# Kernel tuning notes

Hardware: AMD Instinct MI355X
Metric: run time of the kernel (lower is better)

The kernel has to match this reference:

```python
import jax, jax.numpy as jnp
import numpy as np

B, L, H, TD = 384, 64, 300, 64   # batch, seq_len, encoder_size, tracking_lstm_dim
T = 2 * (L - 1)                  # L-1 shifts interleaved with L-1 reduces (valid tree)


def setup_inputs() -> dict:
    key = jax.random.key(0)
    ks = jax.random.split(key, 9)

    def w(k, shape):
        fan_in = shape[-1]
        return jax.random.normal(k, shape, jnp.float32) * (2.0 / fan_in) ** 0.5

    sequence = jax.random.normal(ks[0], (B, L, 2 * H), jnp.float32)
    # valid transition sequences: odd steps shift (1), even steps reduce left(2)/right(3)
    rng = np.random.default_rng(0)
    tr = np.empty((B, T), dtype=np.int32)
    tr[:, 0::2] = 1
    tr[:, 1::2] = rng.integers(2, 4, size=(B, T // 2))
    return {
        "sequence": sequence,
        "transitions": jnp.asarray(tr),
        # DependencyTreeLSTMCell params (5 gates each)
        "W_c": w(ks[1], (5 * H, TD)),    # input (tracking) -> gates, no bias
        "Uh_w": w(ks[2], (5 * H, H)),    # U_head (with bias)
        "Uh_b": jnp.zeros((5 * H,), jnp.float32),
        "Ul_w": w(ks[3], (5 * H, H)),    # U_child_left, no bias
        "Ur_w": w(ks[4], (5 * H, H)),    # U_child_right, no bias
        # tracking nn.LSTMCell params (torch gate order i,f,g,o)
        "W_ih": w(ks[5], (4 * TD, 3 * H)),
        "W_hh": w(ks[6], (4 * TD, TD)),
        "b_ih": jnp.zeros((4 * TD,), jnp.float32),
        "b_hh": jnp.zeros((4 * TD,), jnp.float32),
        # original code initializes the tracking state with torch.randn
        "th0": jax.random.normal(ks[7], (B, TD), jnp.float32),
        "tc0": jax.random.normal(ks[8], (B, TD), jnp.float32),
    }


def _encode(sequence, transitions, W_c, Uh_w, Uh_b, Ul_w, Ur_w,
            W_ih, W_hh, b_ih, b_hh, th0, tc0):
    Bz, Lz, D2 = sequence.shape
    Hz = D2 // 2
    tokens_h, tokens_c = sequence[..., :Hz], sequence[..., Hz:]
    bidx = jnp.arange(Bz)
    S = Lz + 1  # max stack depth
    stack_h = jnp.zeros((Bz, S, Hz), sequence.dtype)
    stack_h = stack_h.at[:, 0].set(tokens_h[:, 0]).at[:, 1].set(tokens_h[:, 0])
    stack_c = jnp.zeros((Bz, S, Hz), sequence.dtype)
    stack_c = stack_c.at[:, 0].set(tokens_c[:, 0]).at[:, 1].set(tokens_c[:, 0])
    sp = jnp.full((Bz,), 2, jnp.int32)   # stack pointer (stack seeded with token 0 twice)
    bp = jnp.zeros((Bz,), jnp.int32)     # buffer pointer (buffer NOT popped by the seed)

    def step(carry, trans):
        stack_h, stack_c, sp, bp, th, tc = carry
        buf_h = tokens_h[bidx, bp]
        buf_c = tokens_c[bidx, bp]
        s1_h = stack_h[bidx, sp - 1]
        s2_h = stack_h[bidx, sp - 2]
        s1_c = stack_c[bidx, sp - 1]
        s2_c = stack_c[bidx, sp - 2]
        # tracking LSTMCell on [buffer_top, stack_top, stack_second]
        x = jnp.concatenate([buf_h, s1_h, s2_h], axis=1)          # (B, 3H)
        g = x @ W_ih.T + b_ih + th @ W_hh.T + b_hh                # (B, 4*TD)
        i_t, f_t, g_t, o_t = jnp.split(g, 4, axis=1)
        tc = jax.nn.sigmoid(f_t) * tc + jax.nn.sigmoid(i_t) * jnp.tanh(g_t)
        th = jax.nn.sigmoid(o_t) * jnp.tanh(tc)
        # composition. NOTE: the original cell does `h_child, c_child = hc_head`,
        # so only the HEAD state enters the gate math -- replicated faithfully.
        is_left = trans == 2
        is_red = is_left | (trans == 3)
        lm = is_left[:, None]
        h_head = jnp.where(lm, s1_h, s2_h)   # left-arc: head is the stack top
        c_head = jnp.where(lm, s1_c, s2_c)
        u_dir = jnp.where(lm, h_head @ Ul_w.T, h_head @ Ur_w.T)
        gates = h_head @ Uh_w.T + Uh_b + u_dir + th @ W_c.T       # (B, 5H)
        i_j, o_j, f_jh, f_jc, u_j = jnp.split(gates, 5, axis=1)
        c_j = (jax.nn.sigmoid(i_j) * jnp.tanh(u_j)
               + jax.nn.sigmoid(f_jh) * c_head
               + jax.nn.sigmoid(f_jc) * c_head)  # c_child aliases c_head in original
        h_j = jax.nn.sigmoid(o_j) * jnp.tanh(c_j)
        # stack update: shift pushes buffer top at sp; reduce pops 2, writes at sp-2
        rm = is_red[:, None]
        wpos = jnp.where(is_red, sp - 2, sp)
        stack_h = stack_h.at[bidx, wpos].set(jnp.where(rm, h_j, buf_h))
        stack_c = stack_c.at[bidx, wpos].set(jnp.where(rm, c_j, buf_c))
        sp = jnp.where(is_red, sp - 1, sp + 1)
        bp = bp + (trans == 1).astype(bp.dtype)
        return (stack_h, stack_c, sp, bp, th, tc), None

    init = (stack_h, stack_c, sp, bp, th0, tc0)
    (stack_h, stack_c, sp, bp, th, tc), _ = jax.lax.scan(step, init, transitions.T)
    return stack_h[bidx, sp - 1]   # (B, H): hidden state of each stack top


def reference(sequence, transitions, W_c, Uh_w, Uh_b, Ul_w, Ur_w,
              W_ih, W_hh, b_ih, b_hh, th0, tc0):
    return _encode(sequence, transitions, W_c, Uh_w, Uh_b, Ul_w, Ur_w,
                   W_ih, W_hh, b_ih, b_hh, th0, tc0)
```

## Files before the change

### kernel.cpp

```cpp
#include <hip/hip_runtime.h>
#include <stdint.h>

#define BB 384
#define LSEQ 64
#define HH 300
#define TDIM 64
#define TT 126
#define NP 63
#define KP 320
#define G4 256
#define G5 1500
#define SEQB 38400

typedef unsigned int u32;
typedef unsigned short ush;
typedef float f32x4 __attribute__((ext_vector_type(4)));
typedef short bf16x8 __attribute__((ext_vector_type(8)));

__device__ __forceinline__ float sigm(float x){ return 1.0f/(1.0f + expf(-x)); }
__device__ __forceinline__ ush f2bf(float x){ u32 u = __float_as_uint(x); u32 r = u + 0x7fff + ((u>>16)&1); return (ush)(r>>16); }
__device__ __forceinline__ float bf2f(ush h){ return __uint_as_float(((u32)h)<<16); }
__device__ __forceinline__ bf16x8 ld16(const ush* p){ return *reinterpret_cast<const bf16x8*>(p); }
__device__ __forceinline__ void mfma16(f32x4& d, bf16x8 a, bf16x8 b){
    d = __builtin_amdgcn_mfma_f32_16x16x32_bf16(a, b, d, 0, 0, 0);
}

__global__ void k_wprep(const float* __restrict__ Uh, const float* __restrict__ Ul,
                        const float* __restrict__ Ur, const float* __restrict__ Wih,
                        const float* __restrict__ Whh,
                        const float* __restrict__ bih, const float* __restrict__ bhh,
                        ush* ULh, ush* ULl, ush* URh, ush* URl,
                        ush* WihH, ush* WihL, ush* WhhH, ush* WhhL, float* bsum)
{
    int i0 = blockIdx.x*blockDim.x + threadIdx.x;
    int stride = gridDim.x*blockDim.x;
    for (int i = i0; i < G5*KP; i += stride) {
        int j = i / KP, k = i - j*KP;
        float vl = 0.f, vr = 0.f;
        if (k < HH) { float u = Uh[j*HH+k]; vl = u + Ul[j*HH+k]; vr = u + Ur[j*HH+k]; }
        ush h;
        h = f2bf(vl); ULh[i] = h; ULl[i] = f2bf(vl - bf2f(h));
        h = f2bf(vr); URh[i] = h; URl[i] = f2bf(vr - bf2f(h));
    }
    for (int i = i0; i < G4*3*KP; i += stride) {
        int j = i / (3*KP), kk = i - j*(3*KP);
        int part = kk / KP, k = kk - part*KP;
        float v = (k < HH) ? Wih[j*900 + part*HH + k] : 0.f;
        ush h = f2bf(v); WihH[i] = h; WihL[i] = f2bf(v - bf2f(h));
    }
    for (int i = i0; i < G4*TDIM; i += stride) {
        float v = Whh[i]; ush h = f2bf(v); WhhH[i] = h; WhhL[i] = f2bf(v - bf2f(h));
    }
    for (int i = i0; i < G4; i += stride) bsum[i] = bih[i] + bhh[i];
}

__global__ void k_cvt(const float* __restrict__ seq, ush* tokH, ush* tokL)
{
    int i0 = blockIdx.x*blockDim.x + threadIdx.x;
    int stride = gridDim.x*blockDim.x;
    for (int i = i0; i < BB*LSEQ*KP; i += stride) {
        int bt = i / KP, k = i - bt*KP;
        int b = bt >> 6, t = bt & 63;
        float v = (k < HH) ? seq[b*SEQB + t*600 + k] : 0.f;
        ush h = f2bf(v); tokH[i] = h; tokL[i] = f2bf(v - bf2f(h));
    }
}

__global__ void k_init(const float* __restrict__ seq, const float* __restrict__ th0,
                       const float* __restrict__ tc0, const ush* __restrict__ tokH,
                       const ush* __restrict__ tokL,
                       ush* accH, ush* accL, float* acc_c, float* acc_h,
                       ush* thH, ush* thL, float* tc_buf)
{
    int i0 = blockIdx.x*blockDim.x + threadIdx.x;
    int stride = gridDim.x*blockDim.x;
    for (int i = i0; i < BB*KP; i += stride) {
        int b = i / KP, k = i - b*KP;
        accH[i] = tokH[b*LSEQ*KP + k]; accL[i] = tokL[b*LSEQ*KP + k];
    }
    for (int i = i0; i < BB*HH; i += stride) {
        int b = i / HH, c = i - b*HH;
        acc_c[i] = seq[b*SEQB + HH + c];
        acc_h[i] = seq[b*SEQB + c];
    }
    for (int i = i0; i < BB*TDIM; i += stride) {
        float v = th0[i]; ush h = f2bf(v);
        thH[i] = h; thL[i] = f2bf(v - bf2f(h));
        tc_buf[i] = tc0[i];
    }
}

__global__ __launch_bounds__(448) void k_prep2(const int* __restrict__ trans, int* perm, int* rbarr)
{
    int p = blockIdx.x, t = threadIdx.x;
    __shared__ int cl, cr, rb;
    if (t == 0) { cl = 0; cr = 0; }
    __syncthreads();
    int isleft = 0;
    if (t < BB) {
        isleft = (trans[t*TT + 2*p + 1] == 2);
        if (isleft) atomicAdd(&cl, 1); else atomicAdd(&cr, 1);
    }
    __syncthreads();
    if (t == 0) { rb = ((cl + 63) >> 6) << 6; rbarr[p] = rb; cl = 0; cr = 0; }
    __syncthreads();
    perm[p*448 + t] = -1;
    __syncthreads();
    if (t < BB) {
        int slot = isleft ? atomicAdd(&cl, 1) : rb + atomicAdd(&cr, 1);
        perm[p*448 + slot] = t;
    }
}

__global__ __launch_bounds__(256) void k_pairA(int p,
    const ush* __restrict__ tokH, const ush* __restrict__ tokL,
    const ush* __restrict__ accHp, const ush* __restrict__ accLp,
    const ush* __restrict__ thHp, const ush* __restrict__ thLp,
    const ush* __restrict__ ULh, const ush* __restrict__ ULl,
    const ush* __restrict__ URh, const ush* __restrict__ URl,
    const ush* __restrict__ WihH, const ush* __restrict__ WihL,
    const ush* __restrict__ WhhH, const ush* __restrict__ WhhL,
    const int* __restrict__ perm, const int* __restrict__ rbarr,
    float* __restrict__ gbufE, float* __restrict__ gbufO, float* __restrict__ Pbuf)
{
    const int bid = blockIdx.x, tid = threadIdx.x;
    const int w = tid >> 6, lane = tid & 63;
    const int l15 = lane & 15, kg = lane >> 4;
    f32x4 acc[4];
    #pragma unroll
    for (int cf = 0; cf < 4; ++cf) acc[cf] = (f32x4){0.f,0.f,0.f,0.f};

    if (bid < 48) {
        const int seg = (bid >= 24);
        const int q = bid - seg*24;
        const int rt = q >> 2, ct = q & 3;
        const int r0 = rt*64, c0 = ct*64;
        const int b = r0 + w*16 + l15;
        const ush* aH[3]; const ush* aL[3];
        if (!seg) {
            aH[0] = tokH + (b*64 + p)*KP;   aL[0] = tokL + (b*64 + p)*KP;
            aH[1] = accHp + b*KP;           aL[1] = accLp + b*KP;
            aH[2] = tokH + (b*64)*KP;       aL[2] = tokL + (b*64)*KP;
        } else {
            aH[0] = tokH + (b*64 + p+1)*KP; aL[0] = tokL + (b*64 + p+1)*KP;
            aH[1] = tokH + (b*64 + p)*KP;   aL[1] = tokL + (b*64 + p)*KP;
            aH[2] = accHp + b*KP;           aL[2] = accLp + b*KP;
        }
        const ush* bH[4]; const ush* bL[4];
        #pragma unroll
        for (int cf = 0; cf < 4; ++cf) {
            int j = c0 + cf*16 + l15;
            bH[cf] = WihH + j*(3*KP) + kg*8;
            bL[cf] = WihL + j*(3*KP) + kg*8;
        }
        #pragma unroll
        for (int part = 0; part < 3; ++part) {
            const ush* pah = aH[part] + kg*8;
            const ush* pal = aL[part] + kg*8;
            const int ko = part*KP;
            #pragma unroll
            for (int kc = 0; kc < KP; kc += 32) {
                bf16x8 ah = ld16(pah + kc);
                bf16x8 al = ld16(pal + kc);
                bf16x8 b0 = ld16(bH[0]+ko+kc), b1 = ld16(bH[1]+ko+kc), b2 = ld16(bH[2]+ko+kc), b3 = ld16(bH[3]+ko+kc);
                bf16x8 c0v = ld16(bL[0]+ko+kc), c1 = ld16(bL[1]+ko+kc), c2 = ld16(bL[2]+ko+kc), c3 = ld16(bL[3]+ko+kc);
                mfma16(acc[0],ah,b0); mfma16(acc[1],ah,b1); mfma16(acc[2],ah,b2); mfma16(acc[3],ah,b3);
                mfma16(acc[0],al,b0); mfma16(acc[1],al,b1); mfma16(acc[2],al,b2); mfma16(acc[3],al,b3);
                mfma16(acc[0],ah,c0v); mfma16(acc[1],ah,c1); mfma16(acc[2],ah,c2); mfma16(acc[3],ah,c3);
            }
        }
        if (!seg) {
            const ush* pah = thHp + b*TDIM + kg*8;
            const ush* pal = thLp + b*TDIM + kg*8;
            #pragma unroll
            for (int kc = 0; kc < 64; kc += 32) {
                bf16x8 ah = ld16(pah + kc);
                bf16x8 al = ld16(pal + kc);
                #pragma unroll
                for (int cf = 0; cf < 4; ++cf) {
                    int j = c0 + cf*16 + l15;
                    bf16x8 bh = ld16(WhhH + j*TDIM + kg*8 + kc);
                    bf16x8 bl = ld16(WhhL + j*TDIM + kg*8 + kc);
                    mfma16(acc[cf], ah, bh);
                    mfma16(acc[cf], al, bh);
                    mfma16(acc[cf], ah, bl);
                }
            }
        }
        float* out = seg ? gbufO : gbufE;
        #pragma unroll
        for (int r = 0; r < 4; ++r) {
            int row = r0 + w*16 + kg*4 + r;
            #pragma unroll
            for (int cf = 0; cf < 4; ++cf) {
                int col = c0 + cf*16 + l15;
                out[row*G4 + col] = acc[cf][r];
            }
        }
    } else {
        const int q = bid - 48;
        const int rt = q / 24, ct = q - rt*24;
        const int s0 = rt*64, c0 = ct*64;
        const int* pp = perm + p*448;
        if (pp[s0] < 0) return;
        const int RB = rbarr[p];
        const bool left = (s0 < RB);
        int ar = pp[s0 + w*16 + l15]; if (ar < 0) ar = 0;
        const ush* pah = (left ? tokH + (ar*64 + p)*KP : accHp + ar*KP) + kg*8;
        const ush* pal = (left ? tokL + (ar*64 + p)*KP : accLp + ar*KP) + kg*8;
        const ush* WBh = left ? ULh : URh;
        const ush* WBl = left ? ULl : URl;
        const ush* bH[4]; const ush* bL[4];
        #pragma unroll
        for (int cf = 0; cf < 4; ++cf) {
            int j = c0 + cf*16 + l15; if (j > G5-1) j = G5-1;
            bH[cf] = WBh + j*KP + kg*8;
            bL[cf] = WBl + j*KP + kg*8;
        }
        #pragma unroll
        for (int kc = 0; kc < KP; kc += 32) {
            bf16x8 ah = ld16(pah + kc);
            bf16x8 al = ld16(pal + kc);
            bf16x8 b0 = ld16(bH[0]+kc), b1 = ld16(bH[1]+kc), b2 = ld16(bH[2]+kc), b3 = ld16(bH[3]+kc);
            bf16x8 c0v = ld16(bL[0]+kc), c1 = ld16(bL[1]+kc), c2 = ld16(bL[2]+kc), c3 = ld16(bL[3]+kc);
            mfma16(acc[0],ah,b0); mfma16(acc[1],ah,b1); mfma16(acc[2],ah,b2); mfma16(acc[3],ah,b3);
            mfma16(acc[0],al,b0); mfma16(acc[1],al,b1); mfma16(acc[2],al,b2); mfma16(acc[3],al,b3);
            mfma16(acc[0],ah,c0v); mfma16(acc[1],ah,c1); mfma16(acc[2],ah,c2); mfma16(acc[3],ah,c3);
        }
        #pragma unroll
        for (int r = 0; r < 4; ++r) {
            int pr = pp[s0 + w*16 + kg*4 + r];
            if (pr < 0) continue;
            #pragma unroll
            for (int cf = 0; cf < 4; ++cf) {
                int col = c0 + cf*16 + l15;
                if (col < G5) Pbuf[pr*G5 + col] = acc[cf][r];
            }
        }
    }
}

__global__ __launch_bounds__(256) void k_pairB(int p,
    const float* __restrict__ seq, const int* __restrict__ trans,
    const float* __restrict__ Whh, const float* __restrict__ Wc,
    const float* __restrict__ Uhb, const float* __restrict__ bsum,
    const float* __restrict__ gbufE, const float* __restrict__ gbufO,
    const float* __restrict__ Pbuf,
    ush* __restrict__ thH, ush* __restrict__ thL, float* __restrict__ tc_buf,
    float* __restrict__ acc_c, float* __restrict__ acc_h,
    ush* __restrict__ accHp, ush* __restrict__ accLp)
{
    __shared__ __align__(16) float thl[4][64], tcl[4][64], gel[4][256];
    __shared__ __align__(16) float g5l[4][G5];
    const int tid = threadIdx.x;
    const int r0 = blockIdx.x*4;
    const int row = tid >> 6, d = tid & 63;
    const int b = r0 + row;

    {
        float gi = gbufE[b*G4 + d]        + bsum[d];
        float gf = gbufE[b*G4 + 64 + d]   + bsum[64 + d];
        float gg = gbufE[b*G4 + 128 + d]  + bsum[128 + d];
        float go = gbufE[b*G4 + 192 + d]  + bsum[192 + d];
        float tcp = tc_buf[b*TDIM + d];
        float tce = sigm(gf)*tcp + sigm(gi)*tanhf(gg);
        float the = sigm(go)*tanhf(tce);
        thl[row][d] = the; tcl[row][d] = tce;
    }
    __syncthreads();
    {
        int j = tid;
        float s[4] = {0.f,0.f,0.f,0.f};
        #pragma unroll
        for (int k = 0; k < 64; k += 4) {
            float4 wv = *(const float4*)&Whh[j*TDIM + k];
            #pragma unroll
            for (int rr = 0; rr < 4; ++rr) {
                float4 t4 = *(const float4*)&thl[rr][k];
                s[rr] += t4.x*wv.x + t4.y*wv.y + t4.z*wv.z + t4.w*wv.w;
            }
        }
        float bs = bsum[j];
        #pragma unroll
        for (int rr = 0; rr < 4; ++rr)
            gel[rr][j] = gbufO[(r0+rr)*G4 + j] + bs + s[rr];
    }
    __syncthreads();
    {
        float gi = gel[row][d], gf = gel[row][64+d], gg = gel[row][128+d], go = gel[row][192+d];
        float tco = sigm(gf)*tcl[row][d] + sigm(gi)*tanhf(gg);
        float tho = sigm(go)*tanhf(tco);
        tc_buf[b*TDIM + d] = tco;
        ush h = f2bf(tho);
        thH[b*TDIM + d] = h; thL[b*TDIM + d] = f2bf(tho - bf2f(h));
        __syncthreads();
        thl[row][d] = tho;
    }
    __syncthreads();
    for (int c = tid; c < G5; c += 256) {
        float s[4] = {0.f,0.f,0.f,0.f};
        #pragma unroll
        for (int k = 0; k < 64; k += 4) {
            float4 wv = *(const float4*)&Wc[c*TDIM + k];
            #pragma unroll
            for (int rr = 0; rr < 4; ++rr) {
                float4 t4 = *(const float4*)&thl[rr][k];
                s[rr] += t4.x*wv.x + t4.y*wv.y + t4.z*wv.z + t4.w*wv.w;
            }
        }
        float ub = Uhb[c];
        #pragma unroll
        for (int rr = 0; rr < 4; ++rr)
            g5l[rr][c] = Pbuf[(r0+rr)*G5 + c] + ub + s[rr];
    }
    __syncthreads();
    for (int idx = tid; idx < 4*HH; idx += 256) {
        int rr = idx / HH, c = idx - rr*HH;
        int bb = r0 + rr;
        bool left = (trans[bb*TT + 2*p + 1] == 2);
        float ch = left ? seq[bb*SEQB + p*600 + HH + c] : acc_c[bb*HH + c];
        float gi = g5l[rr][c], go = g5l[rr][HH+c], gfh = g5l[rr][2*HH+c], gfc = g5l[rr][3*HH+c], gu = g5l[rr][4*HH+c];
        float cj = sigm(gi)*tanhf(gu) + (sigm(gfh) + sigm(gfc))*ch;
        float hj = sigm(go)*tanhf(cj);
        acc_c[bb*HH + c] = cj;
        acc_h[bb*HH + c] = hj;
        ush h = f2bf(hj);
        accHp[bb*KP + c] = h; accLp[bb*KP + c] = f2bf(hj - bf2f(h));
    }
}

__global__ void k_out(const float* __restrict__ acc_h, float* __restrict__ out)
{
    int i = blockIdx.x*blockDim.x + threadIdx.x;
    if (i < BB*HH) out[i] = acc_h[i];
}

extern "C" void kernel_launch(void* const* d_in, const int* in_sizes, int n_in,
                              void* d_out, int out_size, void* d_ws, size_t ws_size,
                              hipStream_t stream)
{
    const float* seq  = (const float*)d_in[0];
    const int*   trans= (const int*)d_in[1];
    const float* Wc   = (const float*)d_in[2];
    const float* Uhw  = (const float*)d_in[3];
    const float* Uhb  = (const float*)d_in[4];
    const float* Ulw  = (const float*)d_in[5];
    const float* Urw  = (const float*)d_in[6];
    const float* Wih  = (const float*)d_in[7];
    const float* Whh  = (const float*)d_in[8];
    const float* bih  = (const float*)d_in[9];
    const float* bhh  = (const float*)d_in[10];
    const float* th0  = (const float*)d_in[11];
    const float* tc0  = (const float*)d_in[12];
    float* out = (float*)d_out;

    char* w = (char*)d_ws;
    size_t off = 0;
    auto alloc = [&](size_t nbytes) {
        void* ptr = w + off;
        off = (off + nbytes + 255) & ~(size_t)255;
        return ptr;
    };
    ush* tokH = (ush*)alloc((size_t)BB*LSEQ*KP*2);
    ush* tokL = (ush*)alloc((size_t)BB*LSEQ*KP*2);
    ush* accH = (ush*)alloc((size_t)BB*KP*2);
    ush* accL = (ush*)alloc((size_t)BB*KP*2);
    ush* ULh  = (ush*)alloc((size_t)G5*KP*2);
    ush* ULl  = (ush*)alloc((size_t)G5*KP*2);
    ush* URh  = (ush*)alloc((size_t)G5*KP*2);
    ush* URl  = (ush*)alloc((size_t)G5*KP*2);
    ush* WihH = (ush*)alloc((size_t)G4*3*KP*2);
    ush* WihL = (ush*)alloc((size_t)G4*3*KP*2);
    ush* WhhH = (ush*)alloc((size_t)G4*TDIM*2);
    ush* WhhL = (ush*)alloc((size_t)G4*TDIM*2);
    ush* thH  = (ush*)alloc((size_t)BB*TDIM*2);
    ush* thL  = (ush*)alloc((size_t)BB*TDIM*2);
    float* bsum  = (float*)alloc((size_t)G4*4);
    float* gbufE = (float*)alloc((size_t)BB*G4*4);
    float* gbufO = (float*)alloc((size_t)BB*G4*4);
    float* Pbuf  = (float*)alloc((size_t)BB*G5*4);
    float* tcb   = (float*)alloc((size_t)BB*TDIM*4);
    float* acc_c = (float*)alloc((size_t)BB*HH*4);
    float* acc_h = (float*)alloc((size_t)BB*HH*4);
    int* perm  = (int*)alloc((size_t)NP*448*4);
    int* rbarr = (int*)alloc((size_t)NP*4);

    k_wprep<<<960, 256, 0, stream>>>(Uhw, Ulw, Urw, Wih, Whh, bih, bhh,
                                     ULh, ULl, URh, URl, WihH, WihL, WhhH, WhhL, bsum);
    k_cvt<<<2048, 256, 0, stream>>>(seq, tokH, tokL);
    k_init<<<512, 256, 0, stream>>>(seq, th0, tc0, tokH, tokL,
                                    accH, accL, acc_c, acc_h, thH, thL, tcb);
    k_prep2<<<NP, 448, 0, stream>>>(trans, perm, rbarr);

    for (int p = 0; p < NP; ++p) {
        k_pairA<<<216, 256, 0, stream>>>(p, tokH, tokL, accH, accL, thH, thL,
                                         ULh, ULl, URh, URl, WihH, WihL, WhhH, WhhL,
                                         perm, rbarr, gbufE, gbufO, Pbuf);
        k_pairB<<<96, 256, 0, stream>>>(p, seq, trans, Whh, Wc, Uhb, bsum,
                                        gbufE, gbufO, Pbuf,
                                        thH, thL, tcb, acc_c, acc_h, accH, accL);
    }
    k_out<<<(BB*HH + 255)/256, 256, 0, stream>>>(acc_h, out);
}
```

Baseline: 4.255 ms.

## Fuse per-step kernel pairs into one persistent kernel with grid barriers

Replaces the 126 per-step kernel launches (pairA/pairB for each of 63 pairs) with a single persistent kernel of 216 blocks that loops over steps and synchronises with an atomic-counter grid barrier. The aim is to remove launch overhead and inter-kernel gaps on the sequential recurrence. The risk is that it relies on all 216 blocks being co-resident, and spin-wait barriers add their own latency. Shared memory for the elementwise phase is now allocated in every block, which may reduce occupancy.

```diff
diff --git a/kernel.cpp b/kernel.cpp
--- a/kernel.cpp
+++ b/kernel.cpp
@@ -11,6 +11,7 @@
 #define G4 256
 #define G5 1500
 #define SEQB 38400
+#define NBLK 216
 
 typedef unsigned int u32;
 typedef unsigned short ush;
@@ -23,6 +24,18 @@
 __device__ __forceinline__ bf16x8 ld16(const ush* p){ return *reinterpret_cast<const bf16x8*>(p); }
 __device__ __forceinline__ void mfma16(f32x4& d, bf16x8 a, bf16x8 b){
     d = __builtin_amdgcn_mfma_f32_16x16x32_bf16(a, b, d, 0, 0, 0);
+}
+
+__device__ __forceinline__ void gbar(int* cnt, int target) {
+    __syncthreads();
+    if (threadIdx.x == 0) {
+        __threadfence();
+        __hip_atomic_fetch_add(cnt, 1, __ATOMIC_RELEASE, __HIP_MEMORY_SCOPE_AGENT);
+        while (__hip_atomic_load(cnt, __ATOMIC_ACQUIRE, __HIP_MEMORY_SCOPE_AGENT) < target)
+            __builtin_amdgcn_s_sleep(2);
+        __threadfence();
+    }
+    __syncthreads();
 }
 
 __global__ void k_wprep(const float* __restrict__ Uh, const float* __restrict__ Ul,
@@ -90,9 +103,11 @@
     }
 }
 
-__global__ __launch_bounds__(448) void k_prep2(const int* __restrict__ trans, int* perm, int* rbarr)
+__global__ __launch_bounds__(448) void k_prep2(const int* __restrict__ trans, int* perm, int* rbarr,
+                                               int* bar)
 {
     int p = blockIdx.x, t = threadIdx.x;
+    if (p == 0 && t == 0) *bar = 0;
     __shared__ int cl, cr, rb;
     if (t == 0) { cl = 0; cr = 0; }
     __syncthreads();
@@ -112,220 +127,227 @@
     }
 }
 
-__global__ __launch_bounds__(256) void k_pairA(int p,
-    const ush* __restrict__ tokH, const ush* __restrict__ tokL,
-    const ush* __restrict__ accHp, const ush* __restrict__ accLp,
-    const ush* __restrict__ thHp, const ush* __restrict__ thLp,
-    const ush* __restrict__ ULh, const ush* __restrict__ ULl,
-    const ush* __restrict__ URh, const ush* __restrict__ URl,
-    const ush* __restrict__ WihH, const ush* __restrict__ WihL,
-    const ush* __restrict__ WhhH, const ush* __restrict__ WhhL,
-    const int* __restrict__ perm, const int* __restrict__ rbarr,
-    float* __restrict__ gbufE, float* __restrict__ gbufO, float* __restrict__ Pbuf)
+struct Prm {
+    const float* seq; const int* trans;
+    const float* Wc; const float* Uhb; const float* bsum;
+    const ush* tokH; const ush* tokL;
+    ush* accH; ush* accL;
+    ush* thH; ush* thL;
+    float* tcb; float* acc_c; float* acc_h;
+    const ush* ULh; const ush* ULl; const ush* URh; const ush* URl;
+    const ush* WihH; const ush* WihL; const ush* WhhH; const ush* WhhL;
+    const float* Whh;
+    const int* perm; const int* rbarr;
+    float* gbufE; float* gbufO; float* Pbuf;
+    int* bar;
+};
+
+__global__ __launch_bounds__(256) void k_persist(Prm pr)
 {
     const int bid = blockIdx.x, tid = threadIdx.x;
     const int w = tid >> 6, lane = tid & 63;
     const int l15 = lane & 15, kg = lane >> 4;
-    f32x4 acc[4];
-    #pragma unroll
-    for (int cf = 0; cf < 4; ++cf) acc[cf] = (f32x4){0.f,0.f,0.f,0.f};
-
-    if (bid < 48) {
-        const int seg = (bid >= 24);
-        const int q = bid - seg*24;
-        const int rt = q >> 2, ct = q & 3;
-        const int r0 = rt*64, c0 = ct*64;
-        const int b = r0 + w*16 + l15;
-        const ush* aH[3]; const ush* aL[3];
-        if (!seg) {
-            aH[0] = tokH + (b*64 + p)*KP;   aL[0] = tokL + (b*64 + p)*KP;
-            aH[1] = accHp + b*KP;           aL[1] = accLp + b*KP;
-            aH[2] = tokH + (b*64)*KP;       aL[2] = tokL + (b*64)*KP;
-        } else {
-            aH[0] = tokH + (b*64 + p+1)*KP; aL[0] = tokL + (b*64 + p+1)*KP;
-            aH[1] = tokH + (b*64 + p)*KP;   aL[1] = tokL + (b*64 + p)*KP;
-            aH[2] = accHp + b*KP;           aL[2] = accLp + b*KP;
-        }
-        const ush* bH[4]; const ush* bL[4];
-        #pragma unroll
-        for (int cf = 0; cf < 4; ++cf) {
-            int j = c0 + cf*16 + l15;
-            bH[cf] = WihH + j*(3*KP) + kg*8;
-            bL[cf] = WihL + j*(3*KP) + kg*8;
-        }
-        #pragma unroll
-        for (int part = 0; part < 3; ++part) {
-            const ush* pah = aH[part] + kg*8;
-            const ush* pal = aL[part] + kg*8;
-            const int ko = part*KP;
+
+    __shared__ __align__(16) float thl[4][64], tcl[4][64], gel[4][256];
+    __shared__ __align__(16) float g5l[4][G5];
+
+    int btgt = 0;
+    for (int p = 0; p < NP; ++p) {
+        if (bid < 48) {
+            const int seg = (bid >= 24);
+            const int q = bid - seg*24;
+            const int rt = q >> 2, ct = q & 3;
+            const int r0 = rt*64, c0 = ct*64;
+            const int b = r0 + w*16 + l15;
+            f32x4 acc[4];
             #pragma unroll
-            for (int kc = 0; kc < KP; kc += 32) {
-                bf16x8 ah = ld16(pah + kc);
-                bf16x8 al = ld16(pal + kc);
-                bf16x8 b0 = ld16(bH[0]+ko+kc), b1 = ld16(bH[1]+ko+kc), b2 = ld16(bH[2]+ko+kc), b3 = ld16(bH[3]+ko+kc);
-                bf16x8 c0v = ld16(bL[0]+ko+kc), c1 = ld16(bL[1]+ko+kc), c2 = ld16(bL[2]+ko+kc), c3 = ld16(bL[3]+ko+kc);
-                mfma16(acc[0],ah,b0); mfma16(acc[1],ah,b1); mfma16(acc[2],ah,b2); mfma16(acc[3],ah,b3);
-                mfma16(acc[0],al,b0); mfma16(acc[1],al,b1); mfma16(acc[2],al,b2); mfma16(acc[3],al,b3);
-                mfma16(acc[0],ah,c0v); mfma16(acc[1],ah,c1); mfma16(acc[2],ah,c2); mfma16(acc[3],ah,c3);
-            }
-        }
-        if (!seg) {
-            const ush* pah = thHp + b*TDIM + kg*8;
-            const ush* pal = thLp + b*TDIM + kg*8;
-            #pragma unroll
-            for (int kc = 0; kc < 64; kc += 32) {
-                bf16x8 ah = ld16(pah + kc);
-                bf16x8 al = ld16(pal + kc);
-                #pragma unroll
-                for (int cf = 0; cf < 4; ++cf) {
-                    int j = c0 + cf*16 + l15;
-                    bf16x8 bh = ld16(WhhH + j*TDIM + kg*8 + kc);
-                    bf16x8 bl = ld16(WhhL + j*TDIM + kg*8 + kc);
-                    mfma16(acc[cf], ah, bh);
-                    mfma16(acc[cf], al, bh);
-                    mfma16(acc[cf], ah, bl);
-                }
-            }
-        }
-        float* out = seg ? gbufO : gbufE;
-        #pragma unroll
-        for (int r = 0; r < 4; ++r) {
-            int row = r0 + w*16 + kg*4 + r;
+            for (int cf = 0; cf < 4; ++cf) acc[cf] = (f32x4){0.f,0.f,0.f,0.f};
+            const ush* aH[3]; const ush* aL[3];
+            if (!seg) {
+                aH[0] = pr.tokH + (b*64 + p)*KP;   aL[0] = pr.tokL + (b*64 + p)*KP;
+                aH[1] = pr.accH + b*KP;            aL[1] = pr.accL + b*KP;
+                aH[2] = pr.tokH + (b*64)*KP;       aL[2] = pr.tokL + (b*64)*KP;
+            } else {
+                aH[0] = pr.tokH + (b*64 + p+1)*KP; aL[0] = pr.tokL + (b*64 + p+1)*KP;
+                aH[1] = pr.tokH + (b*64 + p)*KP;   aL[1] = pr.tokL + (b*64 + p)*KP;
+                aH[2] = pr.accH + b*KP;            aL[2] = pr.accL + b*KP;
+            }
+            const ush* bH[4]; const ush* bL[4];
             #pragma unroll
             for (int cf = 0; cf < 4; ++cf) {
-                int col = c0 + cf*16 + l15;
-                out[row*G4 + col] = acc[cf][r];
+                int j = c0 + cf*16 + l15;
+                bH[cf] = pr.WihH + j*(3*KP) + kg*8;
+                bL[cf] = pr.WihL + j*(3*KP) + kg*8;
+            }
+            #pragma unroll
+            for (int part = 0; part < 3; ++part) {
+                const ush* pah = aH[part] + kg*8;
+                const ush* pal = aL[part] + kg*8;
+                const int ko = part*KP;
+                #pragma unroll
+                for (int kc = 0; kc < KP; kc += 32) {
+                    bf16x8 ah = ld16(pah + kc);
+                    bf16x8 al = ld16(pal + kc);
+                    bf16x8 b0 = ld16(bH[0]+ko+kc), b1 = ld16(bH[1]+ko+kc), b2 = ld16(bH[2]+ko+kc), b3 = ld16(bH[3]+ko+kc);
+                    bf16x8 c0v = ld16(bL[0]+ko+kc), c1 = ld16(bL[1]+ko+kc), c2 = ld16(bL[2]+ko+kc), c3 = ld16(bL[3]+ko+kc);
+                    mfma16(acc[0],ah,b0); mfma16(acc[1],ah,b1); mfma16(acc[2],ah,b2); mfma16(acc[3],ah,b3);
+                    mfma16(acc[0],al,b0); mfma16(acc[1],al,b1); mfma16(acc[2],al,b2); mfma16(acc[3],al,b3);
+                    mfma16(acc[0],ah,c0v); mfma16(acc[1],ah,c1); mfma16(acc[2],ah,c2); mfma16(acc[3],ah,c3);
+                }
+            }
+            if (!seg) {
+                const ush* pah = pr.thH + b*TDIM + kg*8;
+                const ush* pal = pr.thL + b*TDIM + kg*8;
+                #pragma unroll
+                for (int kc = 0; kc < 64; kc += 32) {
+                    bf16x8 ah = ld16(pah + kc);
+                    bf16x8 al = ld16(pal + kc);
+                    #pragma unroll
+                    for (int cf = 0; cf < 4; ++cf) {
+                        int j = c0 + cf*16 + l15;
+                        bf16x8 bh = ld16(pr.WhhH + j*TDIM + kg*8 + kc);
+                        bf16x8 bl = ld16(pr.WhhL + j*TDIM + kg*8 + kc);
+                        mfma16(acc[cf], ah, bh);
+                        mfma16(acc[cf], al, bh);
+                        mfma16(acc[cf], ah, bl);
+                    }
+                }
+            }
+            float* out = seg ? pr.gbufO : pr.gbufE;
+            #pragma unroll
+            for (int r = 0; r < 4; ++r) {
+                int row = r0 + w*16 + kg*4 + r;
+                #pragma unroll
+                for (int cf = 0; cf < 4; ++cf) {
+                    int col = c0 + cf*16 + l15;
+                    out[row*G4 + col] = acc[cf][r];
+                }
+            }
+        } else {
+            const int q = bid - 48;
+            const int rt = q / 24, ct = q - rt*24;
+            const int s0 = rt*64, c0 = ct*64;
+            const int* pp = pr.perm + p*448;
+            if (pp[s0] >= 0) {
+                const int RB = pr.rbarr[p];
+                const bool left = (s0 < RB);
+                f32x4 acc[4];
+                #pragma unroll
+                for (int cf = 0; cf < 4; ++cf) acc[cf] = (f32x4){0.f,0.f,0.f,0.f};
+                int ar = pp[s0 + w*16 + l15]; if (ar < 0) ar = 0;
+                const ush* pah = (left ? pr.tokH + (ar*64 + p)*KP : pr.accH + ar*KP) + kg*8;
+                const ush* pal = (left ? pr.tokL + (ar*64 + p)*KP : pr.accL + ar*KP) + kg*8;
+                const ush* WBh = left ? pr.ULh : pr.URh;
+                const ush* WBl = left ? pr.ULl : pr.URl;
+                const ush* bH[4]; const ush* bL[4];
+                #pragma unroll
+                for (int cf = 0; cf < 4; ++cf) {
+                    int j = c0 + cf*16 + l15; if (j > G5-1) j = G5-1;
+                    bH[cf] = WBh + j*KP + kg*8;
+                    bL[cf] = WBl + j*KP + kg*8;
+                }
+                #pragma unroll
+                for (int kc = 0; kc < KP; kc += 32) {
+                    bf16x8 ah = ld16(pah + kc);
+                    bf16x8 al = ld16(pal + kc);
+                    bf16x8 b0 = ld16(bH[0]+kc), b1 = ld16(bH[1]+kc), b2 = ld16(bH[2]+kc), b3 = ld16(bH[3]+kc);
+                    bf16x8 c0v = ld16(bL[0]+kc), c1 = ld16(bL[1]+kc), c2 = ld16(bL[2]+kc), c3 = ld16(bL[3]+kc);
+                    mfma16(acc[0],ah,b0); mfma16(acc[1],ah,b1); mfma16(acc[2],ah,b2); mfma16(acc[3],ah,b3);
+                    mfma16(acc[0],al,b0); mfma16(acc[1],al,b1); mfma16(acc[2],al,b2); mfma16(acc[3],al,b3);
+                    mfma16(acc[0],ah,c0v); mfma16(acc[1],ah,c1); mfma16(acc[2],ah,c2); mfma16(acc[3],ah,c3);
+                }
+                #pragma unroll
+                for (int r = 0; r < 4; ++r) {
+                    int prw = pp[s0 + w*16 + kg*4 + r];
+                    if (prw < 0) continue;
+                    #pragma unroll
+                    for (int cf = 0; cf < 4; ++cf) {
+                        int col = c0 + cf*16 + l15;
+                        if (col < G5) pr.Pbuf[prw*G5 + col] = acc[cf][r];
+                    }
+                }
             }
         }
-    } else {
-        const int q = bid - 48;
-        const int rt = q / 24, ct = q - rt*24;
-        const int s0 = rt*64, c0 = ct*64;
-        const int* pp = perm + p*448;
-        if (pp[s0] < 0) return;
-        const int RB = rbarr[p];
-        const bool left = (s0 < RB);
-        int ar = pp[s0 + w*16 + l15]; if (ar < 0) ar = 0;
-        const ush* pah = (left ? tokH + (ar*64 + p)*KP : accHp + ar*KP) + kg*8;
-        const ush* pal = (left ? tokL + (ar*64 + p)*KP : accLp + ar*KP) + kg*8;
-        const ush* WBh = left ? ULh : URh;
-        const ush* WBl = left ? ULl : URl;
-        const ush* bH[4]; const ush* bL[4];
-        #pragma unroll
-        for (int cf = 0; cf < 4; ++cf) {
-            int j = c0 + cf*16 + l15; if (j > G5-1) j = G5-1;
-            bH[cf] = WBh + j*KP + kg*8;
-            bL[cf] = WBl + j*KP + kg*8;
+        btgt += NBLK;
+        gbar(pr.bar, btgt);
+
+        if (bid < 96) {
+            const int r0 = bid*4;
+            const int row = tid >> 6, d = tid & 63;
+            const int b = r0 + row;
+            {
+                float gi = pr.gbufE[b*G4 + d]        + pr.bsum[d];
+                float gf = pr.gbufE[b*G4 + 64 + d]   + pr.bsum[64 + d];
+                float gg = pr.gbufE[b*G4 + 128 + d]  + pr.bsum[128 + d];
+                float go = pr.gbufE[b*G4 + 192 + d]  + pr.bsum[192 + d];
+                float tcp = pr.tcb[b*TDIM + d];
+                float tce = sigm(gf)*tcp + sigm(gi)*tanhf(gg);
+                float the = sigm(go)*tanhf(tce);
+                thl[row][d] = the; tcl[row][d] = tce;
+            }
+            __syncthreads();
+            {
+                int j = tid;
+                float s[4] = {0.f,0.f,0.f,0.f};
+                #pragma unroll
+                for (int k = 0; k < 64; k += 4) {
+                    float4 wv = *(const float4*)&pr.Whh[j*TDIM + k];
+                    #pragma unroll
+                    for (int rr = 0; rr < 4; ++rr) {
+                        float4 t4 = *(const float4*)&thl[rr][k];
+                        s[rr] += t4.x*wv.x + t4.y*wv.y + t4.z*wv.z + t4.w*wv.w;
+                    }
+                }
+                float bs = pr.bsum[j];
+                #pragma unroll
+                for (int rr = 0; rr < 4; ++rr)
+                    gel[rr][j] = pr.gbufO[(r0+rr)*G4 + j] + bs + s[rr];
+            }
+            __syncthreads();
+            {
+                float gi = gel[row][d], gf = gel[row][64+d], gg = gel[row][128+d], go = gel[row][192+d];
+                float tco = sigm(gf)*tcl[row][d] + sigm(gi)*tanhf(gg);
+                float tho = sigm(go)*tanhf(tco);
+                pr.tcb[b*TDIM + d] = tco;
+                ush h = f2bf(tho);
+                pr.thH[b*TDIM + d] = h; pr.thL[b*TDIM + d] = f2bf(tho - bf2f(h));
+                __syncthreads();
+                thl[row][d] = tho;
+            }
+            __syncthreads();
+            for (int c = tid; c < G5; c += 256) {
+                float s[4] = {0.f,0.f,0.f,0.f};
+                #pragma unroll
+                for (int k = 0; k < 64; k += 4) {
+                    float4 wv = *(const float4*)&pr.Wc[c*TDIM + k];
+                    #pragma unroll
+                    for (int rr = 0; rr < 4; ++rr) {
+                        float4 t4 = *(const float4*)&thl[rr][k];
+                        s[rr] += t4.x*wv.x + t4.y*wv.y + t4.z*wv.z + t4.w*wv.w;
+                    }
+                }
+                float ub = pr.Uhb[c];
+                #pragma unroll
+                for (int rr = 0; rr < 4; ++rr)
+                    g5l[rr][c] = pr.Pbuf[(r0+rr)*G5 + c] + ub + s[rr];
+            }
+            __syncthreads();
+            for (int idx = tid; idx < 4*HH; idx += 256) {
+                int rr = idx / HH, c = idx - rr*HH;
+                int bb = r0 + rr;
+                bool left = (pr.trans[bb*TT + 2*p + 1] == 2);
+                float ch = left ? pr.seq[bb*SEQB + p*600 + HH + c] : pr.acc_c[bb*HH + c];
+                float gi = g5l[rr][c], go = g5l[rr][HH+c], gfh = g5l[rr][2*HH+c], gfc = g5l[rr][3*HH+c], gu = g5l[rr][4*HH+c];
+                float cj = sigm(gi)*tanhf(gu) + (sigm(gfh) + sigm(gfc))*ch;
+                float hj = sigm(go)*tanhf(cj);
+                pr.acc_c[bb*HH + c] = cj;
+                pr.acc_h[bb*HH + c] = hj;
+                ush h = f2bf(hj);
+                pr.accH[bb*KP + c] = h; pr.accL[bb*KP + c] = f2bf(hj - bf2f(h));
+            }
         }
-        #pragma unroll
-        for (int kc = 0; kc < KP; kc += 32) {
-            bf16x8 ah = ld16(pah + kc);
-            bf16x8 al = ld16(pal + kc);
-            bf16x8 b0 = ld16(bH[0]+kc), b1 = ld16(bH[1]+kc), b2 = ld16(bH[2]+kc), b3 = ld16(bH[3]+kc);
-            bf16x8 c0v = ld16(bL[0]+kc), c1 = ld16(bL[1]+kc), c2 = ld16(bL[2]+kc), c3 = ld16(bL[3]+kc);
-            mfma16(acc[0],ah,b0); mfma16(acc[1],ah,b1); mfma16(acc[2],ah,b2); mfma16(acc[3],ah,b3);
-            mfma16(acc[0],al,b0); mfma16(acc[1],al,b1); mfma16(acc[2],al,b2); mfma16(acc[3],al,b3);
-            mfma16(acc[0],ah,c0v); mfma16(acc[1],ah,c1); mfma16(acc[2],ah,c2); mfma16(acc[3],ah,c3);
-        }
-        #pragma unroll
-        for (int r = 0; r < 4; ++r) {
-            int pr = pp[s0 + w*16 + kg*4 + r];
-            if (pr < 0) continue;
-            #pragma unroll
-            for (int cf = 0; cf < 4; ++cf) {
-                int col = c0 + cf*16 + l15;
-                if (col < G5) Pbuf[pr*G5 + col] = acc[cf][r];
-            }
-        }
-    }
-}
-
-__global__ __launch_bounds__(256) void k_pairB(int p,
-    const float* __restrict__ seq, const int* __restrict__ trans,
-    const float* __restrict__ Whh, const float* __restrict__ Wc,
-    const float* __restrict__ Uhb, const float* __restrict__ bsum,
-    const float* __restrict__ gbufE, const float* __restrict__ gbufO,
-    const float* __restrict__ Pbuf,
-    ush* __restrict__ thH, ush* __restrict__ thL, float* __restrict__ tc_buf,
-    float* __restrict__ acc_c, float* __restrict__ acc_h,
-    ush* __restrict__ accHp, ush* __restrict__ accLp)
-{
-    __shared__ __align__(16) float thl[4][64], tcl[4][64], gel[4][256];
-    __shared__ __align__(16) float g5l[4][G5];
-    const int tid = threadIdx.x;
-    const int r0 = blockIdx.x*4;
-    const int row = tid >> 6, d = tid & 63;
-    const int b = r0 + row;
-
-    {
-        float gi = gbufE[b*G4 + d]        + bsum[d];
-        float gf = gbufE[b*G4 + 64 + d]   + bsum[64 + d];
-        float gg = gbufE[b*G4 + 128 + d]  + bsum[128 + d];
-        float go = gbufE[b*G4 + 192 + d]  + bsum[192 + d];
-        float tcp = tc_buf[b*TDIM + d];
-        float tce = sigm(gf)*tcp + sigm(gi)*tanhf(gg);
-        float the = sigm(go)*tanhf(tce);
-        thl[row][d] = the; tcl[row][d] = tce;
-    }
-    __syncthreads();
-    {
-        int j = tid;
-        float s[4] = {0.f,0.f,0.f,0.f};
-        #pragma unroll
-        for (int k = 0; k < 64; k += 4) {
-            float4 wv = *(const float4*)&Whh[j*TDIM + k];
-            #pragma unroll
-            for (int rr = 0; rr < 4; ++rr) {
-                float4 t4 = *(const float4*)&thl[rr][k];
-                s[rr] += t4.x*wv.x + t4.y*wv.y + t4.z*wv.z + t4.w*wv.w;
-            }
-        }
-        float bs = bsum[j];
-        #pragma unroll
-        for (int rr = 0; rr < 4; ++rr)
-            gel[rr][j] = gbufO[(r0+rr)*G4 + j] + bs + s[rr];
-    }
-    __syncthreads();
-    {
-        float gi = gel[row][d], gf = gel[row][64+d], gg = gel[row][128+d], go = gel[row][192+d];
-        float tco = sigm(gf)*tcl[row][d] + sigm(gi)*tanhf(gg);
-        float tho = sigm(go)*tanhf(tco);
-        tc_buf[b*TDIM + d] = tco;
-        ush h = f2bf(tho);
-        thH[b*TDIM + d] = h; thL[b*TDIM + d] = f2bf(tho - bf2f(h));
-        __syncthreads();
-        thl[row][d] = tho;
-    }
-    __syncthreads();
-    for (int c = tid; c < G5; c += 256) {
-        float s[4] = {0.f,0.f,0.f,0.f};
-        #pragma unroll
-        for (int k = 0; k < 64; k += 4) {
-            float4 wv = *(const float4*)&Wc[c*TDIM + k];
-            #pragma unroll
-            for (int rr = 0; rr < 4; ++rr) {
-                float4 t4 = *(const float4*)&thl[rr][k];
-                s[rr] += t4.x*wv.x + t4.y*wv.y + t4.z*wv.z + t4.w*wv.w;
-            }
-        }
-        float ub = Uhb[c];
-        #pragma unroll
-        for (int rr = 0; rr < 4; ++rr)
-            g5l[rr][c] = Pbuf[(r0+rr)*G5 + c] + ub + s[rr];
-    }
-    __syncthreads();
-    for (int idx = tid; idx < 4*HH; idx += 256) {
-        int rr = idx / HH, c = idx - rr*HH;
-        int bb = r0 + rr;
-        bool left = (trans[bb*TT + 2*p + 1] == 2);
-        float ch = left ? seq[bb*SEQB + p*600 + HH + c] : acc_c[bb*HH + c];
-        float gi = g5l[rr][c], go = g5l[rr][HH+c], gfh = g5l[rr][2*HH+c], gfc = g5l[rr][3*HH+c], gu = g5l[rr][4*HH+c];
-        float cj = sigm(gi)*tanhf(gu) + (sigm(gfh) + sigm(gfc))*ch;
-        float hj = sigm(go)*tanhf(cj);
-        acc_c[bb*HH + c] = cj;
-        acc_h[bb*HH + c] = hj;
-        ush h = f2bf(hj);
-        accHp[bb*KP + c] = h; accLp[bb*KP + c] = f2bf(hj - bf2f(h));
+        btgt += NBLK;
+        gbar(pr.bar, btgt);
     }
 }
 
@@ -384,21 +406,30 @@
     float* acc_h = (float*)alloc((size_t)BB*HH*4);
     int* perm  = (int*)alloc((size_t)NP*448*4);
     int* rbarr = (int*)alloc((size_t)NP*4);
+    int* bar   = (int*)alloc((size_t)256);
 
     k_wprep<<<960, 256, 0, stream>>>(Uhw, Ulw, Urw, Wih, Whh, bih, bhh,
                                      ULh, ULl, URh, URl, WihH, WihL, WhhH, WhhL, bsum);
     k_cvt<<<2048, 256, 0, stream>>>(seq, tokH, tokL);
     k_init<<<512, 256, 0, stream>>>(seq, th0, tc0, tokH, tokL,
                                     accH, accL, acc_c, acc_h, thH, thL, tcb);
-    k_prep2<<<NP, 448, 0, stream>>>(trans, perm, rbarr);
-
-    for (int p = 0; p < NP; ++p) {
-        k_pairA<<<216, 256, 0, stream>>>(p, tokH, tokL, accH, accL, thH, thL,
-                                         ULh, ULl, URh, URl, WihH, WihL, WhhH, WhhL,
-                                         perm, rbarr, gbufE, gbufO, Pbuf);
-        k_pairB<<<96, 256, 0, stream>>>(p, seq, trans, Whh, Wc, Uhb, bsum,
-                                        gbufE, gbufO, Pbuf,
-                                        thH, thL, tcb, acc_c, acc_h, accH, accL);
-    }
+    k_prep2<<<NP, 448, 0, stream>>>(trans, perm, rbarr, bar);
+
+    Prm prm;
+    prm.seq = seq; prm.trans = trans;
+    prm.Wc = Wc; prm.Uhb = Uhb; prm.bsum = bsum;
+    prm.tokH = tokH; prm.tokL = tokL;
+    prm.accH = accH; prm.accL = accL;
+    prm.thH = thH; prm.thL = thL;
+    prm.tcb = tcb; prm.acc_c = acc_c; prm.acc_h = acc_h;
+    prm.ULh = ULh; prm.ULl = ULl; prm.URh = URh; prm.URl = URl;
+    prm.WihH = WihH; prm.WihL = WihL; prm.WhhH = WhhH; prm.WhhL = WhhL;
+    prm.Whh = Whh;
+    prm.perm = perm; prm.rbarr = rbarr;
+    prm.gbufE = gbufE; prm.gbufO = gbufO; prm.Pbuf = Pbuf;
+    prm.bar = bar;
+
+    k_persist<<<NBLK, 256, 0, stream>>>(prm);
+
     k_out<<<(BB*HH + 255)/256, 256, 0, stream>>>(acc_h, out);
 }
```

Result: slower. 10.37 ms (+143.7%).
